# Kernel optimization log

Hardware: AMD Instinct MI355X
Metric: run time of the kernel (lower is better)

The kernel has to match this reference:

```python
import jax, jax.numpy as jnp
import numpy as np

N, D, C_CLS = 8192, 512, 1000
SCALE = 1.0
LOW_THRE = 1.0 / C_CLS
EPS = 1e-12  # torch F.normalize eps


def _l2norm(x):
    n = jnp.sqrt(jnp.sum(x * x, axis=1, keepdims=True))
    return x / jnp.maximum(n, EPS)


def setup_inputs() -> dict:
    key = jax.random.key(0)
    k1, k2, k3, k4, k5 = jax.random.split(key, 5)
    feature = jax.random.normal(k1, (N, D), jnp.float32)
    proxy_raw = jax.random.normal(k2, (C_CLS, D), jnp.float32) * 0.02
    cP_weight = jax.random.normal(k3, (D, D), jnp.float32) * 0.05
    # probability-like rows (sum to 1), as prob_detach is a detached softmax output
    prob_detach = jax.nn.softmax(4.0 * jax.random.normal(k4, (N, C_CLS), jnp.float32), axis=-1)
    conf_mask = jax.random.randint(k5, (N,), 0, 2) > 0
    return {"feature": feature, "proxy_raw": proxy_raw, "cP_weight": cP_weight,
            "prob_detach": prob_detach, "conf_mask": conf_mask}


def reference(feature, proxy_raw, cP_weight, prob_detach, conf_mask):
    feat = _l2norm(feature)                                   # (N, D)
    proxy = _l2norm(proxy_raw @ cP_weight.T)                  # (C, D), cP is a linear projection

    class_candidates = prob_detach > LOW_THRE                 # (N, C) bool
    top1_idx = jnp.argmax(prob_detach, axis=1)                # (N,)
    top1_class = jnp.arange(C_CLS)[None, :] == top1_idx[:, None]  # (N, C) bool one-hot

    not_conf = ~conf_mask
    pred_class = (class_candidates & not_conf[:, None]) | (top1_class & conf_mask[:, None])  # (N, C)

    # sc_proxy: (sc_weight.unsqueeze(2) * proxy).sum(dim=1) == matmul
    sc_weight = prob_detach * class_candidates                # (N, C)
    sc_proxy = sc_weight @ proxy                              # (N, D)
    sc_sim = jnp.sum(feat * sc_proxy, axis=1)                 # (N,)

    pred = feat @ proxy.T                                     # (N, C)
    proxy_sim = jnp.take_along_axis(pred, top1_idx[:, None], axis=1)[:, 0]  # (N,)
    pos_pair = jnp.where(conf_mask, proxy_sim, sc_sim)        # (N,)

    # intersection.any(dim=2) == (pred_class @ pred_class.T) > 0 (avoids (N,N,C) tensor)
    pc = pred_class.astype(feat.dtype)
    neg_matrix = ~((pc @ pc.T) > 0)                           # (N, N) bool

    sim = feat @ feat.T                                       # (N, N)
    sim = sim * neg_matrix
    neg_pair = jnp.where(sim < 1e-6, -jnp.inf, sim)           # masked_fill

    logits = jnp.concatenate([pos_pair[:, None], neg_pair], axis=1)  # (N, N+1)
    logp = jax.nn.log_softmax(SCALE * logits, axis=1)
    loss = -jnp.mean(logp[:, 0])                              # nll_loss with label 0

    denom = jnp.sum(not_conf)
    sc_count = jnp.sum(class_candidates & not_conf[:, None])
    sc_num = jnp.where(denom > 0,
                       sc_count.astype(jnp.float32) / jnp.maximum(denom, 1).astype(jnp.float32),
                       jnp.float32(0.0))
    return loss, sc_num
```

## Files before the change

kernel.cpp:

```cpp
#include <hip/hip_runtime.h>
#include <hip/hip_bf16.h>

#define N_ROWS 8192
#define DIM 512
#define C_CLSN 1000
#define C_PAD 1024
#define LOW_THRE (1.0f / 1000.0f)

typedef __bf16 bf16x8 __attribute__((ext_vector_type(8)));
typedef float floatx4 __attribute__((ext_vector_type(4)));
typedef unsigned long long ull;
typedef ull ull2 __attribute__((ext_vector_type(2)));


__device__ __forceinline__ void gl_lds16(const void* g, void* l) {
  __builtin_amdgcn_global_load_lds(
      (const __attribute__((address_space(1))) unsigned int*)g,
      (__attribute__((address_space(3))) unsigned int*)l, 16, 0, 0);
}


__global__ __launch_bounds__(1024) void kzp_v14(const int* __restrict__ conf,
                                                int* __restrict__ perm,
                                                int* __restrict__ counters) {
  int tid = threadIdx.x;
  __shared__ int sc[1024];
  __shared__ int sbad, sodd1, seven1, smode;
  if (tid == 0) { sbad = 0; sodd1 = 0; seven1 = 0; }
  __syncthreads();
  for (int i = tid; i < 2048; i += 1024) {
    int v = conf[i];
    if (v != 0 && v != 1) atomicOr(&sbad, 1);
    if (v == 1) { if (i & 1) atomicAdd(&sodd1, 1); else atomicAdd(&seven1, 1); }
  }
  __syncthreads();
  if (tid == 0) {
    int mode = 0;
    if (sbad) mode = 1;
    else if (seven1 > 0 && sodd1 == 0) mode = 2;
    smode = mode;
  }
  __syncthreads();
  int mode = smode;
  int r0 = tid * 8;
  int f[8]; int cnt = 0;
  #pragma unroll
  for (int k = 0; k < 8; ++k) {
    int r = r0 + k;
    bool c;
    if (mode == 1)      c = ((const unsigned char*)conf)[r] != 0;
    else if (mode == 2) c = ((const long long*)conf)[r] != 0;
    else                c = conf[r] != 0;
    f[k] = c ? 1 : 0; cnt += f[k];
  }
  sc[tid] = cnt;
  __syncthreads();
  for (int off = 1; off < 1024; off <<= 1) {
    int v = (tid >= off) ? sc[tid - off] : 0;
    __syncthreads();
    sc[tid] += v;
    __syncthreads();
  }
  int incl = sc[tid];
  int excl = incl - cnt;
  int total = sc[1023];
  if (tid == 0) counters[3] = total;
  int cpos = excl;
  int npos = total + (r0 - excl);
  #pragma unroll
  for (int k = 0; k < 8; ++k) {
    if (f[k]) perm[cpos++] = r0 + k;
    else      perm[npos++] = r0 + k;
  }
}

__global__ __launch_bounds__(256) void kda_v14(const float* __restrict__ prob,
                                               const float* __restrict__ feature,
                                               const int* __restrict__ perm,
                                               const int* __restrict__ counters_ro,
                                               ull* __restrict__ bits,
                                               int* __restrict__ top1a,
                                               int* __restrict__ cnta,
                                               __bf16* __restrict__ featBF,
                                               unsigned char* __restrict__ featF8) {
  int wv = threadIdx.x >> 6, lane = threadIdx.x & 63;
  int p = blockIdx.x * 4 + wv;
  int orig = perm[p];
  bool is_conf = p < counters_ro[3];
  const float4* pr4 = (const float4*)(prob + (size_t)orig * C_CLSN);
  float4 v[4];
  #pragma unroll
  for (int pass = 0; pass < 4; ++pass) {
    int q = pass * 64 + lane;
    v[pass] = (q < 250) ? pr4[q] : make_float4(-1.f, -1.f, -1.f, -1.f);
  }
  float bv = -1e30f; int bidx = 0x7fffffff;
  int cnt = 0;
  ull myword = 0ULL;
  #pragma unroll
  for (int pass = 0; pass < 4; ++pass) {
    int q = pass * 64 + lane;
    bool inb = q < 250;
    float el[4] = {v[pass].x, v[pass].y, v[pass].z, v[pass].w};
    #pragma unroll
    for (int j = 0; j < 4; ++j) {
      float pv = el[j];
      int c = q * 4 + j;
      if (inb && pv > bv) { bv = pv; bidx = c; }
      ull m = __ballot(inb && (pv > LOW_THRE));
      cnt += (int)__popcll(m);
      if (lane == pass * 4 + j) myword = m;
    }
  }
  #pragma unroll
  for (int m = 1; m < 64; m <<= 1) {
    float ov = __shfl_xor(bv, m); int oi = __shfl_xor(bidx, m);
    if (ov > bv || (ov == bv && oi < bidx)) { bv = ov; bidx = oi; }
  }
  int top1 = bidx;
  if (is_conf) {
    int w1 = ((top1 >> 8) << 2) | (top1 & 3);
    myword = (lane == w1) ? (1ULL << ((top1 >> 2) & 63)) : 0ULL;
  }
  if (lane < 16) bits[(size_t)p * 16 + lane] = myword;
  if (lane == 0) {
    top1a[p] = top1;
    cnta[p] = is_conf ? 0 : cnt;
  }
  const float* fr = feature + (size_t)orig * DIM;
  int c0 = lane * 8;
  float4 v0 = *(const float4*)(fr + c0);
  float4 v1 = *(const float4*)(fr + c0 + 4);
  float ss = v0.x*v0.x + v0.y*v0.y + v0.z*v0.z + v0.w*v0.w
           + v1.x*v1.x + v1.y*v1.y + v1.z*v1.z + v1.w*v1.w;
  #pragma unroll
  for (int m = 1; m < 64; m <<= 1) ss += __shfl_xor(ss, m);
  float scl = 1.0f / fmaxf(sqrtf(ss), 1e-12f);
  float x0 = v0.x*scl, x1 = v0.y*scl, x2 = v0.z*scl, x3 = v0.w*scl;
  float x4 = v1.x*scl, x5 = v1.y*scl, x6 = v1.z*scl, x7 = v1.w*scl;
  bf16x8 bvx;
  bvx[0] = (__bf16)x0; bvx[1] = (__bf16)x1; bvx[2] = (__bf16)x2; bvx[3] = (__bf16)x3;
  bvx[4] = (__bf16)x4; bvx[5] = (__bf16)x5; bvx[6] = (__bf16)x6; bvx[7] = (__bf16)x7;
  int g = p >> 4, r = p & 15;
  *(bf16x8*)((char*)featBF + (size_t)g * 16384 + (size_t)lane * 256 + (size_t)r * 16) = bvx;
  int lo = __builtin_amdgcn_cvt_pk_fp8_f32(x0, x1, 0, false);
  lo = __builtin_amdgcn_cvt_pk_fp8_f32(x2, x3, lo, true);
  int hi = __builtin_amdgcn_cvt_pk_fp8_f32(x4, x5, 0, false);
  hi = __builtin_amdgcn_cvt_pk_fp8_f32(x6, x7, hi, true);
  int2 pk; pk.x = lo; pk.y = hi;
  *(int2*)(featF8 + (size_t)g * 8192 + (size_t)lane * 128 + (size_t)r * 8) = pk;
}

__global__ __launch_bounds__(256) void kbc_v14(const float* __restrict__ raw,
                                               const float* __restrict__ cP,
                                               __bf16* __restrict__ proxyBF) {
  int tid = threadIdx.x;
  int c0 = blockIdx.x * 8;
  int d0 = tid, d1 = tid + 256;
  int g = c0 >> 4;
  int r0 = c0 & 15;
  char* pbase = (char*)proxyBF + (size_t)g * 16384;
  if (c0 >= C_CLSN) {
    #pragma unroll
    for (int cc = 0; cc < 8; ++cc) {
      int row = r0 + cc;
      *(__bf16*)(pbase + (size_t)(d0 >> 3) * 256 + row * 16 + (d0 & 7) * 2) = (__bf16)0.f;
      *(__bf16*)(pbase + (size_t)(d1 >> 3) * 256 + row * 16 + (d1 & 7) * 2) = (__bf16)0.f;
    }
    return;
  }
  __shared__ float sraw[8 * DIM];
  __shared__ float red[8 * 256];
  for (int idx = tid; idx < 8 * DIM; idx += 256)
    sraw[idx] = raw[(size_t)c0 * DIM + idx];
  __syncthreads();
  float acc0[8], acc1[8];
  #pragma unroll
  for (int cc = 0; cc < 8; ++cc) { acc0[cc] = 0.f; acc1[cc] = 0.f; }
  for (int k = 0; k < DIM; k += 4) {
    float4 w0 = *(const float4*)&cP[(size_t)d0 * DIM + k];
    float4 w1 = *(const float4*)&cP[(size_t)d1 * DIM + k];
    #pragma unroll
    for (int cc = 0; cc < 8; ++cc) {
      const float* sr = &sraw[cc * DIM + k];
      acc0[cc] += sr[0]*w0.x + sr[1]*w0.y + sr[2]*w0.z + sr[3]*w0.w;
      acc1[cc] += sr[0]*w1.x + sr[1]*w1.y + sr[2]*w1.z + sr[3]*w1.w;
    }
  }
  #pragma unroll
  for (int cc = 0; cc < 8; ++cc)
    red[cc * 256 + tid] = acc0[cc]*acc0[cc] + acc1[cc]*acc1[cc];
  __syncthreads();
  for (int s = 128; s > 0; s >>= 1) {
    if (tid < s)
      #pragma unroll
      for (int cc = 0; cc < 8; ++cc)
        red[cc * 256 + tid] += red[cc * 256 + tid + s];
    __syncthreads();
  }
  #pragma unroll
  for (int cc = 0; cc < 8; ++cc) {
    float scl = 1.0f / fmaxf(sqrtf(red[cc * 256]), 1e-12f);
    int row = r0 + cc;
    *(__bf16*)(pbase + (size_t)(d0 >> 3) * 256 + row * 16 + (d0 & 7) * 2) = (__bf16)(acc0[cc] * scl);
    *(__bf16*)(pbase + (size_t)(d1 >> 3) * 256 + row * 16 + (d1 & 7) * 2) = (__bf16)(acc1[cc] * scl);
  }
}

__global__ __launch_bounds__(512, 4) void kegg_v14(const __bf16* __restrict__ featBF,
                                                   const __bf16* __restrict__ proxyBF,
                                                   const unsigned char* __restrict__ featF8,
                                                   const float* __restrict__ prob,
                                                   const ull* __restrict__ bits,
                                                   const int* __restrict__ perm,
                                                   const int* __restrict__ top1a,
                                                   const int* __restrict__ counters_ro,
                                                   float* __restrict__ scsim,
                                                   float* __restrict__ possim,
                                                   float* __restrict__ S) {
  __shared__ __align__(16) char smem[50176];
  int tid = threadIdx.x;
  int wv = tid >> 6, lane = tid & 63;
  int wi = wv >> 2, wj = wv & 3;
  int lr = lane >> 4, lc = lane & 15;

  floatx4 acc[4][2];
  floatx4 zero = {0.f, 0.f, 0.f, 0.f};
  #pragma unroll
  for (int ti = 0; ti < 4; ++ti)
    #pragma unroll
    for (int tj = 0; tj < 2; ++tj) acc[ti][tj] = zero;

  if (blockIdx.x < 512) {
    int* pO  = (int*)(smem + 32768);
    int* t1r = (int*)(smem + 33280);
    int bi = blockIdx.x >> 3;
    int bj = blockIdx.x & 7;
    const char* A = (const char*)featBF;
    const char* B = (const char*)proxyBF;
    {
      const char* gA = A + (size_t)((bi * 8 + wv) * 16384) + (size_t)lane * 16;
      const char* gB = B + (size_t)((bj * 8 + wv) * 16384) + (size_t)lane * 16;
      gl_lds16(gA, smem + wv * 1024);
      gl_lds16(gB, smem + 8192 + wv * 1024);
    }
    if (tid < 128) { pO[tid] = perm[bi * 128 + tid]; t1r[tid] = top1a[bi * 128 + tid]; }
    __syncthreads();
    for (int it = 0; it < 16; ++it) {
      int sel = it & 1;
      if (it < 15) {
        int kt = (it + 1) * 32;
        const char* gA = A + (size_t)((bi * 8 + wv) * 16384 + kt * 32) + (size_t)lane * 16;
        const char* gB = B + (size_t)((bj * 8 + wv) * 16384 + kt * 32) + (size_t)lane * 16;
        gl_lds16(gA, smem + (sel ^ 1) * 16384 + wv * 1024);
        gl_lds16(gB, smem + (sel ^ 1) * 16384 + 8192 + wv * 1024);
      }
      const char* bA = smem + sel * 16384;
      const char* bB = bA + 8192;
      bf16x8 afr[4], bfr[2];
      #pragma unroll
      for (int ti = 0; ti < 4; ++ti)
        afr[ti] = *(const bf16x8*)(bA + (wi * 4 + ti) * 1024 + lr * 256 + lc * 16);
      #pragma unroll
      for (int tj = 0; tj < 2; ++tj)
        bfr[tj] = *(const bf16x8*)(bB + (wj * 2 + tj) * 1024 + lr * 256 + lc * 16);
      #pragma unroll
      for (int ti = 0; ti < 4; ++ti)
        #pragma unroll
        for (int tj = 0; tj < 2; ++tj)
          acc[ti][tj] = __builtin_amdgcn_mfma_f32_16x16x32_bf16(afr[ti], bfr[tj], acc[ti][tj], 0, 0, 0);
      if (it < 15) __syncthreads();
    }
    #pragma unroll
    for (int ti = 0; ti < 4; ++ti) {
      int ibase = wi * 64 + ti * 16 + lr * 4;
      float rs[4] = {0.f, 0.f, 0.f, 0.f};
      #pragma unroll
      for (int rr = 0; rr < 4; ++rr) {
        int il = ibase + rr;
        int orig = pO[il];
        int t1 = t1r[il];
        const float* prow = prob + (size_t)orig * C_CLSN;
        #pragma unroll
        for (int tj = 0; tj < 2; ++tj) {
          int c = bj * 128 + wj * 32 + tj * 16 + lc;
          float P = acc[ti][tj][rr];
          float pv = (c < C_CLSN) ? prow[c] : 0.f;
          if (pv > LOW_THRE) rs[rr] += pv * P;
          if (c == t1) possim[bi * 128 + il] = P;
        }
      }
      #pragma unroll
      for (int m = 1; m < 16; m <<= 1)
        #pragma unroll
        for (int rr = 0; rr < 4; ++rr) rs[rr] += __shfl_xor(rs[rr], m);
      if (lc == 0) {
        #pragma unroll
        for (int rr = 0; rr < 4; ++rr)
          atomicAdd(&scsim[bi * 128 + ibase + rr], rs[rr]);
      }
    }
    return;
  }

  ull* bsI = (ull*)(smem + 32768);
  ull* bsJ = (ull*)smem;
  int* t1I = (int*)(smem + 49152);
  int* t1J = (int*)(smem + 49664);

  int b = (int)(((long long)(blockIdx.x - 512) * 997) % 2080);
  int bi = 0, rem = b;
  while (rem >= 64 - bi) { rem -= 64 - bi; bi++; }
  int bj = bi + rem;

  int nconf = counters_ro[3];
  bool allcI = (bi * 128 + 128) <= nconf;
  bool allcJ = (bj * 128 + 128) <= nconf;
  int mode = allcJ ? 0 : (allcI ? 1 : 3);

  const char* F = (const char*)featF8;
  {
    const char* gA = F + (size_t)((bi * 8 + wv) * 8192) + (size_t)lane * 16;
    const char* gB = F + (size_t)((bj * 8 + wv) * 8192) + (size_t)lane * 16;
    gl_lds16(gA, smem + wv * 1024);
    gl_lds16(gB, smem + 8192 + wv * 1024);
  }
  if (tid < 128)      t1I[tid]       = top1a[bi * 128 + tid];
  else if (tid < 256) t1J[tid - 128] = top1a[bj * 128 + tid - 128];
  if (mode == 3) {
    #pragma unroll
    for (int e = 0; e < 4; ++e) {
      int flat = tid + e * 512;
      int row = flat & 127, w = flat >> 7;
      bsI[w * 128 + row] = bits[(size_t)(bi * 128 + row) * 16 + w];
    }
  }
  __syncthreads();

  for (int it = 0; it < 8; ++it) {
    int sel = it & 1;
    if (it < 7) {
      int kt = (it + 1) * 64;
      const char* gA = F + (size_t)((bi * 8 + wv) * 8192 + kt * 16) + (size_t)lane * 16;
      const char* gB = F + (size_t)((bj * 8 + wv) * 8192 + kt * 16) + (size_t)lane * 16;
      gl_lds16(gA, smem + (sel ^ 1) * 16384 + wv * 1024);
      gl_lds16(gB, smem + (sel ^ 1) * 16384 + 8192 + wv * 1024);
    }
    const char* bA = smem + sel * 16384;
    const char* bB = bA + 8192;
    #pragma unroll
    for (int ks = 0; ks < 2; ++ks) {
      long a_[4], b_[2];
      #pragma unroll
      for (int ti = 0; ti < 4; ++ti)
        a_[ti] = *(const long*)(bA + (wi * 4 + ti) * 1024 + (ks * 4 + lr) * 128 + lc * 8);
      #pragma unroll
      for (int tj = 0; tj < 2; ++tj)
        b_[tj] = *(const long*)(bB + (wj * 2 + tj) * 1024 + (ks * 4 + lr) * 128 + lc * 8);
      #pragma unroll
      for (int ti = 0; ti < 4; ++ti)
        #pragma unroll
        for (int tj = 0; tj < 2; ++tj)
          acc[ti][tj] = __builtin_amdgcn_mfma_f32_16x16x32_fp8_fp8(a_[ti], b_[tj], acc[ti][tj], 0, 0, 0);
    }
    if (it < 7) __syncthreads();
  }
  __syncthreads();
  if (mode != 0) {
    #pragma unroll
    for (int e = 0; e < 4; ++e) {
      int flat = tid + e * 512;
      int row = flat & 127, w = flat >> 7;
      bsJ[w * 128 + row] = bits[(size_t)(bj * 128 + row) * 16 + w];
    }
  }
  __syncthreads();

  int tJv[2];
  #pragma unroll
  for (int tj = 0; tj < 2; ++tj) tJv[tj] = t1J[wj * 32 + tj * 16 + lc];

  float cs[2] = {0.f, 0.f};
  #pragma unroll
  for (int ti = 0; ti < 4; ++ti) {
    int ibase = wi * 64 + ti * 16 + lr * 4;
    unsigned inter[8];
    if (mode == 0) {
      #pragma unroll
      for (int rr = 0; rr < 4; ++rr) {
        int tI = t1I[ibase + rr];
        #pragma unroll
        for (int tj = 0; tj < 2; ++tj) inter[rr * 2 + tj] = (tI == tJv[tj]);
      }
    } else if (mode == 1) {
      #pragma unroll
      for (int rr = 0; rr < 4; ++rr) {
        int tI = t1I[ibase + rr];
        int w = ((tI >> 8) << 2) | (tI & 3);
        int bb = (tI >> 2) & 63;
        #pragma unroll
        for (int tj = 0; tj < 2; ++tj) {
          ull word = bsJ[w * 128 + wj * 32 + tj * 16 + lc];
          inter[rr * 2 + tj] = (unsigned)((word >> bb) & 1ULL);
        }
      }
    } else {
      #pragma unroll
      for (int q = 0; q < 8; ++q) inter[q] = 0u;
      #pragma unroll
      for (int w = 0; w < 16; ++w) {
        ull2 a01 = *(const ull2*)&bsI[w * 128 + ibase];
        ull2 a23 = *(const ull2*)&bsI[w * 128 + ibase + 2];
        ull aw[4] = {a01[0], a01[1], a23[0], a23[1]};
        ull bw[2];
        #pragma unroll
        for (int tj = 0; tj < 2; ++tj) bw[tj] = bsJ[w * 128 + wj * 32 + tj * 16 + lc];
        #pragma unroll
        for (int rr = 0; rr < 4; ++rr)
          #pragma unroll
          for (int tj = 0; tj < 2; ++tj) {
            ull t = aw[rr] & bw[tj];
            inter[rr * 2 + tj] |= (unsigned)(t | (t >> 32));
          }
      }
    }
    float rs[4] = {0.f, 0.f, 0.f, 0.f};
    #pragma unroll
    for (int rr = 0; rr < 4; ++rr)
      #pragma unroll
      for (int tj = 0; tj < 2; ++tj) {
        float sim = acc[ti][tj][rr];
        sim = fminf(sim, 1.0f);
        float e_ = ((inter[rr * 2 + tj] == 0u) && (sim >= 1e-6f)) ? __expf(sim) : 0.f;
        rs[rr] += e_;
        cs[tj] += e_;
      }
    #pragma unroll
    for (int m = 1; m < 16; m <<= 1)
      #pragma unroll
      for (int rr = 0; rr < 4; ++rr) rs[rr] += __shfl_xor(rs[rr], m);
    if (lc == 0) {
      #pragma unroll
      for (int rr = 0; rr < 4; ++rr)
        atomicAdd(&S[(size_t)bi * 128 + ibase + rr], rs[rr]);
    }
  }
  if (bi != bj) {
    #pragma unroll
    for (int tj = 0; tj < 2; ++tj) {
      cs[tj] += __shfl_xor(cs[tj], 16);
      cs[tj] += __shfl_xor(cs[tj], 32);
    }
    if (lr == 0) {
      #pragma unroll
      for (int tj = 0; tj < 2; ++tj)
        atomicAdd(&S[(size_t)bj * 128 + wj * 32 + tj * 16 + lc], cs[tj]);
    }
  }
}

__global__ __launch_bounds__(1024) void kf_final_v14(const float* __restrict__ possim,
                                                     const float* __restrict__ scsim,
                                                     const float* __restrict__ S,
                                                     const int* __restrict__ cnta,
                                                     const int* __restrict__ counters,
                                                     float* __restrict__ out) {
  __shared__ float red[1024];
  __shared__ int redi[1024];
  int tid = threadIdx.x;
  int nconf = counters[3];
  float local = 0.f;
  int lcnt = 0;
  for (int i = tid; i < N_ROWS; i += 1024) {
    float p = (i < nconf) ? possim[i] : scsim[i];
    p = fminf(fmaxf(p, -1.1f), 1.1f);
    float s = fmaxf(S[i], 0.0f);
    local += logf(expf(p) + s) - p;
    lcnt += cnta[i];
  }
  red[tid] = local;
  redi[tid] = lcnt;
  __syncthreads();
  for (int s = 512; s > 0; s >>= 1) {
    if (tid < s) { red[tid] += red[tid + s]; redi[tid] += redi[tid + s]; }
    __syncthreads();
  }
  if (tid == 0) {
    float loss = red[0] / (float)N_ROWS;
    int denom = N_ROWS - nconf;
    int scc = redi[0];
    float scn = (denom > 0) ? ((float)scc / (float)denom) : 0.f;
    out[0] = loss;
    out[1] = scn;
  }
}

extern "C" void kernel_launch(void* const* d_in, const int* in_sizes, int n_in,
                              void* d_out, int out_size, void* d_ws, size_t ws_size,
                              hipStream_t stream) {
  const float* feature   = (const float*)d_in[0];
  const float* proxy_raw = (const float*)d_in[1];
  const float* cP        = (const float*)d_in[2];
  const float* prob      = (const float*)d_in[3];
  const int*   conf      = (const int*)d_in[4];
  float* out = (float*)d_out;

  size_t need = (size_t)N_ROWS * DIM * 2
              + (size_t)N_ROWS * DIM
              + (size_t)C_PAD * DIM * 2
              + (size_t)N_ROWS * 16 * 8
              + (size_t)N_ROWS * 4
              + (size_t)N_ROWS * 4
              + (size_t)N_ROWS * 4
              + 256
              + (size_t)N_ROWS * 4
              + (size_t)N_ROWS * 4
              + (size_t)N_ROWS * 4;
  if (ws_size < need) return;

  char* ws = (char*)d_ws;
  __bf16* featBF  = (__bf16*)ws;              ws += (size_t)N_ROWS * DIM * 2;
  unsigned char* featF8 = (unsigned char*)ws; ws += (size_t)N_ROWS * DIM;
  __bf16* proxyBF = (__bf16*)ws;              ws += (size_t)C_PAD * DIM * 2;
  ull* bits       = (ull*)ws;                 ws += (size_t)N_ROWS * 16 * 8;
  float* possim   = (float*)ws;               ws += (size_t)N_ROWS * 4;
  float* S        = (float*)ws;               ws += (size_t)N_ROWS * 4;
  float* scsim    = (float*)ws;               ws += (size_t)N_ROWS * 4;
  int* counters   = (int*)ws;                 ws += 256;
  int* perm       = (int*)ws;                 ws += (size_t)N_ROWS * 4;
  int* top1a      = (int*)ws;                 ws += (size_t)N_ROWS * 4;
  int* cnta       = (int*)ws;                 ws += (size_t)N_ROWS * 4;

  hipMemsetAsync(S, 0, (size_t)N_ROWS * 8 + 256, stream);
  kzp_v14<<<1, 1024, 0, stream>>>(conf, perm, counters);
  kda_v14<<<N_ROWS / 4, 256, 0, stream>>>(prob, feature, perm, counters,
                                          bits, top1a, cnta, featBF, featF8);
  kbc_v14<<<C_PAD / 8, 256, 0, stream>>>(proxy_raw, cP, proxyBF);
  kegg_v14<<<512 + 2080, 512, 0, stream>>>(featBF, proxyBF, featF8, prob, bits, perm,
                                           top1a, counters, scsim, possim, S);
  kf_final_v14<<<1, 1024, 0, stream>>>(possim, scsim, S, cnta, counters, out);
}
```

Baseline: 337.1 us.

## Fuse workspace zeroing into prefix kernel and tile block schedule for L2 locality

Removes the separate memset by having the single-block permutation kernel zero the S/scsim/counters region. It also remaps the block indices of the fused GEMM kernel. Proxy-GEMM blocks now vary the row tile fastest. The triangular sim blocks are grouped into 16x16 super-tiles and interleaved across eight groups so that concurrently running blocks share A/B tiles in cache. Zeroing inside a single block adds a little serial work to that kernel.

```diff
diff --git a/kernel.cpp b/kernel.cpp
--- a/kernel.cpp
+++ b/kernel.cpp
@@ -20,10 +20,12 @@
 }
 
 
-__global__ __launch_bounds__(1024) void kzp_v14(const int* __restrict__ conf,
+__global__ __launch_bounds__(1024) void kzp_v16(const int* __restrict__ conf,
                                                 int* __restrict__ perm,
-                                                int* __restrict__ counters) {
+                                                int* __restrict__ counters,
+                                                int* __restrict__ zbase) {
   int tid = threadIdx.x;
+  for (int i = tid; i < 16448; i += 1024) zbase[i] = 0;
   __shared__ int sc[1024];
   __shared__ int sbad, sodd1, seven1, smode;
   if (tid == 0) { sbad = 0; sodd1 = 0; seven1 = 0; }
@@ -74,7 +76,7 @@
   }
 }
 
-__global__ __launch_bounds__(256) void kda_v14(const float* __restrict__ prob,
+__global__ __launch_bounds__(256) void kda_v16(const float* __restrict__ prob,
                                                const float* __restrict__ feature,
                                                const int* __restrict__ perm,
                                                const int* __restrict__ counters_ro,
@@ -151,7 +153,7 @@
   *(int2*)(featF8 + (size_t)g * 8192 + (size_t)lane * 128 + (size_t)r * 8) = pk;
 }
 
-__global__ __launch_bounds__(256) void kbc_v14(const float* __restrict__ raw,
+__global__ __launch_bounds__(256) void kbc_v16(const float* __restrict__ raw,
                                                const float* __restrict__ cP,
                                                __bf16* __restrict__ proxyBF) {
   int tid = threadIdx.x;
@@ -207,7 +209,7 @@
   }
 }
 
-__global__ __launch_bounds__(512, 4) void kegg_v14(const __bf16* __restrict__ featBF,
+__global__ __launch_bounds__(512, 4) void kegg_v16(const __bf16* __restrict__ featBF,
                                                    const __bf16* __restrict__ proxyBF,
                                                    const unsigned char* __restrict__ featF8,
                                                    const float* __restrict__ prob,
@@ -234,8 +236,8 @@
   if (blockIdx.x < 512) {
     int* pO  = (int*)(smem + 32768);
     int* t1r = (int*)(smem + 33280);
-    int bi = blockIdx.x >> 3;
-    int bj = blockIdx.x & 7;
+    int bi = blockIdx.x & 63;
+    int bj = blockIdx.x >> 6;
     const char* A = (const char*)featBF;
     const char* B = (const char*)proxyBF;
     {
@@ -308,10 +310,24 @@
   int* t1I = (int*)(smem + 49152);
   int* t1J = (int*)(smem + 49664);
 
-  int b = (int)(((long long)(blockIdx.x - 512) * 997) % 2080);
-  int bi = 0, rem = b;
-  while (rem >= 64 - bi) { rem -= 64 - bi; bi++; }
-  int bj = bi + rem;
+  int orig_b = (int)blockIdx.x - 512;
+  int b = (orig_b & 7) * 260 + (orig_b >> 3);
+  const int stOff[10] = {0, 136, 392, 648, 784, 1040, 1176, 1432, 1568, 1824};
+  const int stI[10]   = {0, 2, 0, 3, 0, 1, 1, 2, 0, 1};
+  const int stJ[10]   = {0, 3, 1, 3, 2, 1, 3, 2, 3, 2};
+  int s = 9;
+  #pragma unroll
+  for (int k = 9; k >= 1; --k) if (b < stOff[k]) s = k - 1;
+  int w0_ = b - stOff[s];
+  int bi, bj;
+  if (stI[s] == stJ[s]) {
+    int u = 0, rem = w0_;
+    while (rem >= 16 - u) { rem -= 16 - u; u++; }
+    bi = stI[s] * 16 + u; bj = stJ[s] * 16 + u + rem;
+  } else {
+    bi = stI[s] * 16 + (w0_ >> 4);
+    bj = stJ[s] * 16 + (w0_ & 15);
+  }
 
   int nconf = counters_ro[3];
   bool allcI = (bi * 128 + 128) <= nconf;
@@ -459,7 +475,7 @@
   }
 }
 
-__global__ __launch_bounds__(1024) void kf_final_v14(const float* __restrict__ possim,
+__global__ __launch_bounds__(1024) void kf_final_v16(const float* __restrict__ possim,
                                                      const float* __restrict__ scsim,
                                                      const float* __restrict__ S,
                                                      const int* __restrict__ cnta,
@@ -531,12 +547,11 @@
   int* top1a      = (int*)ws;                 ws += (size_t)N_ROWS * 4;
   int* cnta       = (int*)ws;                 ws += (size_t)N_ROWS * 4;
 
-  hipMemsetAsync(S, 0, (size_t)N_ROWS * 8 + 256, stream);
-  kzp_v14<<<1, 1024, 0, stream>>>(conf, perm, counters);
-  kda_v14<<<N_ROWS / 4, 256, 0, stream>>>(prob, feature, perm, counters,
+  kzp_v16<<<1, 1024, 0, stream>>>(conf, perm, counters, (int*)S);
+  kda_v16<<<N_ROWS / 4, 256, 0, stream>>>(prob, feature, perm, counters,
                                           bits, top1a, cnta, featBF, featF8);
-  kbc_v14<<<C_PAD / 8, 256, 0, stream>>>(proxy_raw, cP, proxyBF);
-  kegg_v14<<<512 + 2080, 512, 0, stream>>>(featBF, proxyBF, featF8, prob, bits, perm,
+  kbc_v16<<<C_PAD / 8, 256, 0, stream>>>(proxy_raw, cP, proxyBF);
+  kegg_v16<<<512 + 2080, 512, 0, stream>>>(featBF, proxyBF, featF8, prob, bits, perm,
                                            top1a, counters, scsim, possim, S);
-  kf_final_v14<<<1, 1024, 0, stream>>>(possim, scsim, S, cnta, counters, out);
-}
+  kf_final_v16<<<1, 1024, 0, stream>>>(possim, scsim, S, cnta, counters, out);
+}
```

After: 395.1 us. 1.17x slower.

## Store feature and proxy matrices row-major and zero accumulators in prep kernel

Applied to the files above, without the earlier changes.

The pre-tiled blocked layouts for the bf16/fp8 feature and proxy buffers are replaced with plain row-major storage. The GEMM kernels now stage data with row-based global-to-LDS loads and adjust the LDS read offsets to match. The separate hipMemsetAsync for the S/scsim region is dropped, and the single-block prep kernel zeros that memory instead. This removes one stream operation and gives coalesced full-row writes in the producer kernels, at the cost of a different global load pattern and possible LDS bank effects in the GEMMs.

```diff
diff --git a/kernel.cpp b/kernel.cpp
--- a/kernel.cpp
+++ b/kernel.cpp
@@ -20,10 +20,12 @@
 }
 
 
-__global__ __launch_bounds__(1024) void kzp_v14(const int* __restrict__ conf,
+__global__ __launch_bounds__(1024) void kzp_v17(const int* __restrict__ conf,
                                                 int* __restrict__ perm,
-                                                int* __restrict__ counters) {
+                                                int* __restrict__ counters,
+                                                int* __restrict__ zbase) {
   int tid = threadIdx.x;
+  for (int i = tid; i < 16448; i += 1024) zbase[i] = 0;
   __shared__ int sc[1024];
   __shared__ int sbad, sodd1, seven1, smode;
   if (tid == 0) { sbad = 0; sodd1 = 0; seven1 = 0; }
@@ -74,7 +76,7 @@
   }
 }
 
-__global__ __launch_bounds__(256) void kda_v14(const float* __restrict__ prob,
+__global__ __launch_bounds__(256) void kda_v17(const float* __restrict__ prob,
                                                const float* __restrict__ feature,
                                                const int* __restrict__ perm,
                                                const int* __restrict__ counters_ro,
@@ -141,31 +143,26 @@
   bf16x8 bvx;
   bvx[0] = (__bf16)x0; bvx[1] = (__bf16)x1; bvx[2] = (__bf16)x2; bvx[3] = (__bf16)x3;
   bvx[4] = (__bf16)x4; bvx[5] = (__bf16)x5; bvx[6] = (__bf16)x6; bvx[7] = (__bf16)x7;
-  int g = p >> 4, r = p & 15;
-  *(bf16x8*)((char*)featBF + (size_t)g * 16384 + (size_t)lane * 256 + (size_t)r * 16) = bvx;
+  *(bf16x8*)(featBF + (size_t)p * DIM + c0) = bvx;
   int lo = __builtin_amdgcn_cvt_pk_fp8_f32(x0, x1, 0, false);
   lo = __builtin_amdgcn_cvt_pk_fp8_f32(x2, x3, lo, true);
   int hi = __builtin_amdgcn_cvt_pk_fp8_f32(x4, x5, 0, false);
   hi = __builtin_amdgcn_cvt_pk_fp8_f32(x6, x7, hi, true);
   int2 pk; pk.x = lo; pk.y = hi;
-  *(int2*)(featF8 + (size_t)g * 8192 + (size_t)lane * 128 + (size_t)r * 8) = pk;
-}
-
-__global__ __launch_bounds__(256) void kbc_v14(const float* __restrict__ raw,
+  *(int2*)(featF8 + (size_t)p * DIM + c0) = pk;
+}
+
+__global__ __launch_bounds__(256) void kbc_v17(const float* __restrict__ raw,
                                                const float* __restrict__ cP,
                                                __bf16* __restrict__ proxyBF) {
   int tid = threadIdx.x;
   int c0 = blockIdx.x * 8;
   int d0 = tid, d1 = tid + 256;
-  int g = c0 >> 4;
-  int r0 = c0 & 15;
-  char* pbase = (char*)proxyBF + (size_t)g * 16384;
   if (c0 >= C_CLSN) {
     #pragma unroll
     for (int cc = 0; cc < 8; ++cc) {
-      int row = r0 + cc;
-      *(__bf16*)(pbase + (size_t)(d0 >> 3) * 256 + row * 16 + (d0 & 7) * 2) = (__bf16)0.f;
-      *(__bf16*)(pbase + (size_t)(d1 >> 3) * 256 + row * 16 + (d1 & 7) * 2) = (__bf16)0.f;
+      proxyBF[(size_t)(c0 + cc) * DIM + d0] = (__bf16)0.f;
+      proxyBF[(size_t)(c0 + cc) * DIM + d1] = (__bf16)0.f;
     }
     return;
   }
@@ -201,13 +198,12 @@
   #pragma unroll
   for (int cc = 0; cc < 8; ++cc) {
     float scl = 1.0f / fmaxf(sqrtf(red[cc * 256]), 1e-12f);
-    int row = r0 + cc;
-    *(__bf16*)(pbase + (size_t)(d0 >> 3) * 256 + row * 16 + (d0 & 7) * 2) = (__bf16)(acc0[cc] * scl);
-    *(__bf16*)(pbase + (size_t)(d1 >> 3) * 256 + row * 16 + (d1 & 7) * 2) = (__bf16)(acc1[cc] * scl);
-  }
-}
-
-__global__ __launch_bounds__(512, 4) void kegg_v14(const __bf16* __restrict__ featBF,
+    proxyBF[(size_t)(c0 + cc) * DIM + d0] = (__bf16)(acc0[cc] * scl);
+    proxyBF[(size_t)(c0 + cc) * DIM + d1] = (__bf16)(acc1[cc] * scl);
+  }
+}
+
+__global__ __launch_bounds__(512, 4) void kegg_v17(const __bf16* __restrict__ featBF,
                                                    const __bf16* __restrict__ proxyBF,
                                                    const unsigned char* __restrict__ featF8,
                                                    const float* __restrict__ prob,
@@ -223,6 +219,7 @@
   int wv = tid >> 6, lane = tid & 63;
   int wi = wv >> 2, wj = wv & 3;
   int lr = lane >> 4, lc = lane & 15;
+  int sr_ = lane & 15, sc16 = lane >> 4;
 
   floatx4 acc[4][2];
   floatx4 zero = {0.f, 0.f, 0.f, 0.f};
@@ -238,22 +235,18 @@
     int bj = blockIdx.x & 7;
     const char* A = (const char*)featBF;
     const char* B = (const char*)proxyBF;
-    {
-      const char* gA = A + (size_t)((bi * 8 + wv) * 16384) + (size_t)lane * 16;
-      const char* gB = B + (size_t)((bj * 8 + wv) * 16384) + (size_t)lane * 16;
-      gl_lds16(gA, smem + wv * 1024);
-      gl_lds16(gB, smem + 8192 + wv * 1024);
-    }
+    size_t arow = (size_t)(bi * 128 + wv * 16 + sr_) * 1024 + sc16 * 16;
+    size_t brow = (size_t)(bj * 128 + wv * 16 + sr_) * 1024 + sc16 * 16;
+    gl_lds16(A + arow, smem + wv * 1024);
+    gl_lds16(B + brow, smem + 8192 + wv * 1024);
     if (tid < 128) { pO[tid] = perm[bi * 128 + tid]; t1r[tid] = top1a[bi * 128 + tid]; }
     __syncthreads();
     for (int it = 0; it < 16; ++it) {
       int sel = it & 1;
       if (it < 15) {
-        int kt = (it + 1) * 32;
-        const char* gA = A + (size_t)((bi * 8 + wv) * 16384 + kt * 32) + (size_t)lane * 16;
-        const char* gB = B + (size_t)((bj * 8 + wv) * 16384 + kt * 32) + (size_t)lane * 16;
-        gl_lds16(gA, smem + (sel ^ 1) * 16384 + wv * 1024);
-        gl_lds16(gB, smem + (sel ^ 1) * 16384 + 8192 + wv * 1024);
+        int ktb = (it + 1) * 64;
+        gl_lds16(A + arow + ktb, smem + (sel ^ 1) * 16384 + wv * 1024);
+        gl_lds16(B + brow + ktb, smem + (sel ^ 1) * 16384 + 8192 + wv * 1024);
       }
       const char* bA = smem + sel * 16384;
       const char* bB = bA + 8192;
@@ -319,12 +312,10 @@
   int mode = allcJ ? 0 : (allcI ? 1 : 3);
 
   const char* F = (const char*)featF8;
-  {
-    const char* gA = F + (size_t)((bi * 8 + wv) * 8192) + (size_t)lane * 16;
-    const char* gB = F + (size_t)((bj * 8 + wv) * 8192) + (size_t)lane * 16;
-    gl_lds16(gA, smem + wv * 1024);
-    gl_lds16(gB, smem + 8192 + wv * 1024);
-  }
+  size_t arow = (size_t)(bi * 128 + wv * 16 + sr_) * 512 + sc16 * 16;
+  size_t brow = (size_t)(bj * 128 + wv * 16 + sr_) * 512 + sc16 * 16;
+  gl_lds16(F + arow, smem + wv * 1024);
+  gl_lds16(F + brow, smem + 8192 + wv * 1024);
   if (tid < 128)      t1I[tid]       = top1a[bi * 128 + tid];
   else if (tid < 256) t1J[tid - 128] = top1a[bj * 128 + tid - 128];
   if (mode == 3) {
@@ -340,23 +331,23 @@
   for (int it = 0; it < 8; ++it) {
     int sel = it & 1;
     if (it < 7) {
-      int kt = (it + 1) * 64;
-      const char* gA = F + (size_t)((bi * 8 + wv) * 8192 + kt * 16) + (size_t)lane * 16;
-      const char* gB = F + (size_t)((bj * 8 + wv) * 8192 + kt * 16) + (size_t)lane * 16;
-      gl_lds16(gA, smem + (sel ^ 1) * 16384 + wv * 1024);
-      gl_lds16(gB, smem + (sel ^ 1) * 16384 + 8192 + wv * 1024);
+      int ktb = (it + 1) * 64;
+      gl_lds16(F + arow + ktb, smem + (sel ^ 1) * 16384 + wv * 1024);
+      gl_lds16(F + brow + ktb, smem + (sel ^ 1) * 16384 + 8192 + wv * 1024);
     }
     const char* bA = smem + sel * 16384;
     const char* bB = bA + 8192;
     #pragma unroll
     for (int ks = 0; ks < 2; ++ks) {
       long a_[4], b_[2];
+      int q = ks * 4 + lr;
+      int koff = (q >> 1) * 256 + lc * 16 + (q & 1) * 8;
       #pragma unroll
       for (int ti = 0; ti < 4; ++ti)
-        a_[ti] = *(const long*)(bA + (wi * 4 + ti) * 1024 + (ks * 4 + lr) * 128 + lc * 8);
+        a_[ti] = *(const long*)(bA + (wi * 4 + ti) * 1024 + koff);
       #pragma unroll
       for (int tj = 0; tj < 2; ++tj)
-        b_[tj] = *(const long*)(bB + (wj * 2 + tj) * 1024 + (ks * 4 + lr) * 128 + lc * 8);
+        b_[tj] = *(const long*)(bB + (wj * 2 + tj) * 1024 + koff);
       #pragma unroll
       for (int ti = 0; ti < 4; ++ti)
         #pragma unroll
@@ -459,7 +450,7 @@
   }
 }
 
-__global__ __launch_bounds__(1024) void kf_final_v14(const float* __restrict__ possim,
+__global__ __launch_bounds__(1024) void kf_final_v17(const float* __restrict__ possim,
                                                      const float* __restrict__ scsim,
                                                      const float* __restrict__ S,
                                                      const int* __restrict__ cnta,
@@ -531,12 +522,11 @@
   int* top1a      = (int*)ws;                 ws += (size_t)N_ROWS * 4;
   int* cnta       = (int*)ws;                 ws += (size_t)N_ROWS * 4;
 
-  hipMemsetAsync(S, 0, (size_t)N_ROWS * 8 + 256, stream);
-  kzp_v14<<<1, 1024, 0, stream>>>(conf, perm, counters);
-  kda_v14<<<N_ROWS / 4, 256, 0, stream>>>(prob, feature, perm, counters,
+  kzp_v17<<<1, 1024, 0, stream>>>(conf, perm, counters, (int*)S);
+  kda_v17<<<N_ROWS / 4, 256, 0, stream>>>(prob, feature, perm, counters,
                                           bits, top1a, cnta, featBF, featF8);
-  kbc_v14<<<C_PAD / 8, 256, 0, stream>>>(proxy_raw, cP, proxyBF);
-  kegg_v14<<<512 + 2080, 512, 0, stream>>>(featBF, proxyBF, featF8, prob, bits, perm,
+  kbc_v17<<<C_PAD / 8, 256, 0, stream>>>(proxy_raw, cP, proxyBF);
+  kegg_v17<<<512 + 2080, 512, 0, stream>>>(featBF, proxyBF, featF8, prob, bits, perm,
                                            top1a, counters, scsim, possim, S);
-  kf_final_v14<<<1, 1024, 0, stream>>>(possim, scsim, S, cnta, counters, out);
-}
+  kf_final_v17<<<1, 1024, 0, stream>>>(possim, scsim, S, cnta, counters, out);
+}
```

Result: slower. 344.8 us (+2.3%).
